# Kernel optimization log

Measured on AMD Instinct MI355X. Metric: run time of the kernel, lower is better.

## Reference

```python
import jax, jax.numpy as jnp
import numpy as np

NUM_LAYERS = 2

def setup_inputs() -> dict:
    key = jax.random.key(0)
    ks = jax.random.split(key, 10)
    N, E, V, D, G = 50000, 800000, 100000, 128, 64
    node_ids = jax.random.randint(ks[0], (N,), 0, V)
    edge_index = jax.random.randint(ks[1], (2, E), 0, N)
    batch = jnp.sort(jax.random.randint(ks[2], (N,), 0, G))
    embed = jax.random.normal(ks[3], (V, D), dtype=jnp.float32)
    conv_w = jax.random.normal(ks[4], (NUM_LAYERS, D, D), dtype=jnp.float32) * (1.0 / np.sqrt(D))
    w_ih = jax.random.normal(ks[5], (3 * D, D), dtype=jnp.float32) * (1.0 / np.sqrt(D))
    w_hh = jax.random.normal(ks[6], (3 * D, D), dtype=jnp.float32) * (1.0 / np.sqrt(D))
    b_ih = jax.random.normal(ks[7], (3 * D,), dtype=jnp.float32) * 0.01
    b_hh = jax.random.normal(ks[8], (3 * D,), dtype=jnp.float32) * 0.01
    return {"node_ids": node_ids, "edge_index": edge_index, "batch": batch,
            "num_graphs": 64, "embed": embed, "conv_w": conv_w,
            "w_ih": w_ih, "w_hh": w_hh, "b_ih": b_ih, "b_hh": b_hh}


def _gru_cell(x, h, w_ih, w_hh, b_ih, b_hh):
    # torch.nn.GRUCell math; gate order r, z, n
    gi = x @ w_ih.T + b_ih
    gh = h @ w_hh.T + b_hh
    i_r, i_z, i_n = jnp.split(gi, 3, axis=-1)
    h_r, h_z, h_n = jnp.split(gh, 3, axis=-1)
    r = jax.nn.sigmoid(i_r + h_r)
    z = jax.nn.sigmoid(i_z + h_z)
    n = jnp.tanh(i_n + r * h_n)
    return (1.0 - z) * n + z * h


def reference(node_ids, edge_index, batch, num_graphs, embed, conv_w, w_ih, w_hh, b_ih, b_hh):
    N = node_ids.shape[0]
    src, dst = edge_index[0], edge_index[1]
    h = embed[node_ids]  # [N, D]
    for i in range(NUM_LAYERS):
        m = h @ conv_w[i]                                   # [N, D]
        agg = jax.ops.segment_sum(m[src], dst, num_segments=N)  # scatter-add messages
        h = _gru_cell(agg, h, w_ih, w_hh, b_ih, b_hh)
    # global mean pool per graph
    sums = jax.ops.segment_sum(h, batch, num_segments=num_graphs)       # [G, D]
    counts = jax.ops.segment_sum(jnp.ones((N,), h.dtype), batch, num_segments=num_graphs)
    return sums / jnp.maximum(counts, 1.0)[:, None]
```

## Files before the change

### kernel.cpp

```cpp
#include <hip/hip_runtime.h>
#include <hip/hip_bf16.h>


#define DTHREADS 256

typedef __attribute__((ext_vector_type(8))) short bf16x8;
typedef __attribute__((ext_vector_type(4))) float f32x4;

__device__ __forceinline__ float sigf(float x) { return 1.0f / (1.0f + __expf(-x)); }
__device__ __forceinline__ float tanhfast(float x) { return 1.0f - 2.0f / (1.0f + __expf(2.0f * x)); }

__device__ __forceinline__ unsigned short f2bf_rne(float x) {
  unsigned int u = __float_as_uint(x);
  u += 0x7fff + ((u >> 16) & 1);
  return (unsigned short)(u >> 16);
}
__device__ __forceinline__ float bf2f(unsigned int lo16) {
  return __uint_as_float(lo16 << 16);
}

__global__ __launch_bounds__(DTHREADS) void gather_kernel(
    const float* __restrict__ embed, const int* __restrict__ node_ids,
    unsigned short* __restrict__ hb, int N) {
  int idx = blockIdx.x * DTHREADS + threadIdx.x;
  if (idx >= N * 32) return;
  int n = idx >> 5;
  int c = (idx & 31) * 4;
  int v = node_ids[n];
  float4 val = *(const float4*)&embed[(size_t)v * 128 + c];
  unsigned short b[4] = {f2bf_rne(val.x), f2bf_rne(val.y), f2bf_rne(val.z), f2bf_rne(val.w)};
  *(ushort4*)&hb[(size_t)n * 128 + c] = *(ushort4*)b;
}

#define BSHIFT 7
#define BNODES 128

__global__ __launch_bounds__(DTHREADS) void bucket_hist_kernel(
    const int* __restrict__ dst, int* __restrict__ gcnt, int E, int NB) {
  __shared__ int lc[512];
  int tid = threadIdx.x;
  for (int i = tid; i < NB; i += DTHREADS) lc[i] = 0;
  __syncthreads();
  int base = blockIdx.x * 4096;
  #pragma unroll
  for (int q = 0; q < 16; ++q) {
    int e = base + q * 256 + tid;
    if (e < E) atomicAdd(&lc[dst[e] >> BSHIFT], 1);
  }
  __syncthreads();
  for (int i = tid; i < NB; i += DTHREADS) {
    int c = lc[i];
    if (c) atomicAdd(&gcnt[i], c);
  }
}

__global__ __launch_bounds__(512) void bucket_scan_kernel(
    const int* __restrict__ gcnt, int* __restrict__ ptr, int* __restrict__ cur,
    int* __restrict__ row_ptr, int NB, int N) {
  int tid = threadIdx.x;
  int lane = tid & 63, wv = tid >> 6;
  int v = (tid < NB) ? gcnt[tid] : 0;
  int x = v;
  #pragma unroll
  for (int off = 1; off < 64; off <<= 1) {
    int y = __shfl_up(x, (unsigned)off, 64);
    if (lane >= off) x += y;
  }
  __shared__ int ws[8];
  if (lane == 63) ws[wv] = x;
  __syncthreads();
  int woff = 0;
  for (int w = 0; w < wv; ++w) woff += ws[w];
  int excl = woff + x - v;
  if (tid < NB) { ptr[tid] = excl; cur[tid] = excl; }
  if (tid == 511) { int tot = woff + x; ptr[NB] = tot; row_ptr[N] = tot; }
}

__global__ __launch_bounds__(DTHREADS) void bucket_scatter_kernel(
    const int* __restrict__ src, const int* __restrict__ dst,
    int* __restrict__ cur, unsigned int* __restrict__ ebuf, int E, int NB) {
  __shared__ int lc[512];
  __shared__ int lbs[512];
  int tid = threadIdx.x;
  for (int i = tid; i < NB; i += DTHREADS) lc[i] = 0;
  __syncthreads();
  int base = blockIdx.x * 4096;
  int rank[16];
  #pragma unroll
  for (int q = 0; q < 16; ++q) {
    int e = base + q * 256 + tid;
    if (e < E) rank[q] = atomicAdd(&lc[dst[e] >> BSHIFT], 1);
  }
  __syncthreads();
  for (int i = tid; i < NB; i += DTHREADS) {
    int c = lc[i];
    lbs[i] = c ? atomicAdd(&cur[i], c) : 0;
  }
  __syncthreads();
  #pragma unroll
  for (int q = 0; q < 16; ++q) {
    int e = base + q * 256 + tid;
    if (e < E) {
      int d = dst[e];
      unsigned int pk = (unsigned int)src[e] | ((unsigned int)(d & (BNODES - 1)) << 17);
      ebuf[lbs[d >> BSHIFT] + rank[q]] = pk;
    }
  }
}

__global__ __launch_bounds__(DTHREADS) void bucket_sort_kernel(
    const unsigned int* __restrict__ ebuf, const int* __restrict__ ptr,
    int* __restrict__ row_ptr, int* __restrict__ csr_src, int N) {
  __shared__ int cnt[BNODES];
  __shared__ int sc[BNODES];
  const int tid = threadIdx.x;
  const int b = blockIdx.x;
  const int s = ptr[b], e = ptr[b + 1];
  if (tid < BNODES) cnt[tid] = 0;
  __syncthreads();
  for (int i = s + tid; i < e; i += DTHREADS)
    atomicAdd(&cnt[ebuf[i] >> 17], 1);
  __syncthreads();
  if (tid < BNODES) sc[tid] = cnt[tid];
  __syncthreads();
  #pragma unroll
  for (int off = 1; off < BNODES; off <<= 1) {
    int t = 0;
    if (tid < BNODES && tid >= off) t = sc[tid - off];
    __syncthreads();
    if (tid < BNODES) sc[tid] += t;
    __syncthreads();
  }
  if (tid < BNODES) {
    int excl = sc[tid] - cnt[tid];
    int n = b * BNODES + tid;
    if (n < N) row_ptr[n] = s + excl;
    cnt[tid] = excl;
  }
  __syncthreads();
  for (int i = s + tid; i < e; i += DTHREADS) {
    unsigned int pk = ebuf[i];
    int slot = atomicAdd(&cnt[pk >> 17], 1);
    csr_src[s + slot] = (int)(pk & 0x1FFFFu);
  }
}

__global__ __launch_bounds__(DTHREADS) void pack_w_kernel(
    const float* __restrict__ w, unsigned short* __restrict__ wpk, int J) {
  int f = blockIdx.x * DTHREADS + threadIdx.x;
  if (f >= J * 16) return;
  int l = f & 63;
  int s = (f >> 6) & 3;
  int t = (f >> 8) & 3;
  int jb = f >> 10;
  int j = jb * 64 + t * 16 + (l & 15);
  int kb = s * 32 + (l >> 4) * 8;
  unsigned short o[8];
  #pragma unroll
  for (int i = 0; i < 8; ++i) o[i] = f2bf_rne(w[j * 128 + kb + i]);
  *(uint4*)&wpk[(size_t)f * 8] = *(uint4*)o;
}

__global__ __launch_bounds__(DTHREADS) void pack_wc_kernel(
    const float* __restrict__ conv, const float* __restrict__ w_ih,
    unsigned short* __restrict__ wpk) {
  int id = blockIdx.x * DTHREADS + threadIdx.x;
  if (id >= 384 * 128) return;
  int f = id >> 3, i = id & 7;
  int l = f & 63;
  int s = (f >> 6) & 3;
  int t = (f >> 8) & 3;
  int jb = f >> 10;
  int j = jb * 64 + t * 16 + (l & 15);
  int k = s * 32 + (l >> 4) * 8 + i;
  float acc = 0.f;
  for (int d = 0; d < 128; d += 4) {
    float4 cv = *(const float4*)&conv[k * 128 + d];
    float4 wv = *(const float4*)&w_ih[j * 128 + d];
    acc += cv.x * wv.x + cv.y * wv.y + cv.z * wv.z + cv.w * wv.w;
  }
  wpk[(size_t)f * 8 + i] = f2bf_rne(acc);
}

__global__ __launch_bounds__(DTHREADS) void aggregate_kernel(
    const unsigned short* __restrict__ hb, const int* __restrict__ row_ptr,
    const int* __restrict__ csr_src, unsigned short* __restrict__ agg, int N) {
  int w = (blockIdx.x * DTHREADS + threadIdx.x) >> 6;
  if (w >= N) return;
  int lane = threadIdx.x & 63;
  int g = lane >> 4;
  int c = lane & 15;
  int s = row_ptr[w], e = row_ptr[w + 1];
  float acc[8] = {0.f, 0.f, 0.f, 0.f, 0.f, 0.f, 0.f, 0.f};
  for (int i = s; i < e; i += 16) {
    int idx[4]; bool vl[4]; uint4 d[4];
    #pragma unroll
    for (int q = 0; q < 4; ++q) {
      int ii = i + g + q * 4;
      vl[q] = ii < e;
      idx[q] = csr_src[vl[q] ? ii : s];
    }
    #pragma unroll
    for (int q = 0; q < 4; ++q)
      d[q] = *(const uint4*)&hb[(size_t)idx[q] * 128 + c * 8];
    #pragma unroll
    for (int q = 0; q < 4; ++q) {
      if (vl[q]) {
        const unsigned int* dp = (const unsigned int*)&d[q];
        #pragma unroll
        for (int k = 0; k < 4; ++k) {
          acc[2 * k]     += bf2f(dp[k] & 0xffffu);
          acc[2 * k + 1] += bf2f(dp[k] >> 16);
        }
      }
    }
  }
  #pragma unroll
  for (int q = 0; q < 8; ++q) acc[q] += __shfl_xor(acc[q], 16, 64);
  #pragma unroll
  for (int q = 0; q < 8; ++q) acc[q] += __shfl_xor(acc[q], 32, 64);
  if (g == 0) {
    unsigned int o[4];
    #pragma unroll
    for (int q = 0; q < 4; ++q)
      o[q] = (unsigned int)f2bf_rne(acc[2 * q]) | ((unsigned int)f2bf_rne(acc[2 * q + 1]) << 16);
    *(uint4*)&agg[(size_t)w * 128 + c * 8] = *(uint4*)o;
  }
}

__global__ __launch_bounds__(512, 2) void fused_gru_kernel(
    const unsigned short* __restrict__ aggb, const unsigned short* __restrict__ wpk_wc,
    const unsigned short* __restrict__ wpk_hh, const float* __restrict__ b_ih,
    const float* __restrict__ b_hh, unsigned short* __restrict__ hb,
    int N, int nchunks) {
  __shared__ __align__(16) unsigned short Ag[32 * 128];
  __shared__ __align__(16) unsigned short Hs[32 * 128];
  const int tid = threadIdx.x;
  const int wv = tid >> 6, lane = tid & 63;
  const int lm = lane & 15, quad = lane >> 4;

  bf16x8 BI[3][4], BH[3][4];
  #pragma unroll
  for (int g = 0; g < 3; ++g) {
    int jb = g * 2 + (wv >> 2);
    int t = wv & 3;
    #pragma unroll
    for (int s = 0; s < 4; ++s) {
      size_t f = ((size_t)(jb * 4 + t) * 4 + s) * 64 + lane;
      BI[g][s] = *(const bf16x8*)&wpk_wc[f * 8];
      BH[g][s] = *(const bf16x8*)&wpk_hh[f * 8];
    }
  }

  const int jc = wv * 16 + lm;
  const float bir = b_ih[jc], biz = b_ih[128 + jc], bin_ = b_ih[256 + jc];
  const float bhr = b_hh[jc], bhz = b_hh[128 + jc], bhn = b_hh[256 + jc];
  const int c0 = jc >> 3, ej = jc & 7;

  const int srow = tid >> 4, scol = tid & 15;
  const int sdc = (scol ^ (srow & 15)) * 8;

  int ci = blockIdx.x;
  uint4 va = make_uint4(0, 0, 0, 0), vh = make_uint4(0, 0, 0, 0);
  if (ci < nchunks) {
    int n = ci * 32 + srow;
    if (n < N) {
      va = *(const uint4*)&aggb[(size_t)n * 128 + scol * 8];
      vh = *(const uint4*)&hb[(size_t)n * 128 + scol * 8];
    }
  }

  for (; ci < nchunks; ci += gridDim.x) {
    *(uint4*)&Ag[srow * 128 + sdc] = va;
    *(uint4*)&Hs[srow * 128 + sdc] = vh;
    __syncthreads();

    int cn = ci + gridDim.x;
    va = make_uint4(0, 0, 0, 0); vh = make_uint4(0, 0, 0, 0);
    if (cn < nchunks) {
      int n = cn * 32 + srow;
      if (n < N) {
        va = *(const uint4*)&aggb[(size_t)n * 128 + scol * 8];
        vh = *(const uint4*)&hb[(size_t)n * 128 + scol * 8];
      }
    }

    f32x4 accI[2][3], accH[2][3];
    #pragma unroll
    for (int mi = 0; mi < 2; ++mi)
      #pragma unroll
      for (int g = 0; g < 3; ++g) {
        accI[mi][g] = (f32x4){0.f, 0.f, 0.f, 0.f};
        accH[mi][g] = (f32x4){0.f, 0.f, 0.f, 0.f};
      }

    #pragma unroll
    for (int s = 0; s < 4; ++s) {
      bf16x8 afA[2], afH[2];
      #pragma unroll
      for (int mi = 0; mi < 2; ++mi) {
        int m = mi * 16 + lm;
        int chunk = (s * 4 + quad) ^ (m & 15);
        afA[mi] = *(const bf16x8*)&Ag[m * 128 + chunk * 8];
        afH[mi] = *(const bf16x8*)&Hs[m * 128 + chunk * 8];
      }
      #pragma unroll
      for (int g = 0; g < 3; ++g)
        #pragma unroll
        for (int mi = 0; mi < 2; ++mi) {
          accI[mi][g] = __builtin_amdgcn_mfma_f32_16x16x32_bf16(afA[mi], BI[g][s], accI[mi][g], 0, 0, 0);
          accH[mi][g] = __builtin_amdgcn_mfma_f32_16x16x32_bf16(afH[mi], BH[g][s], accH[mi][g], 0, 0, 0);
        }
    }

    const int n0 = ci * 32;
    #pragma unroll
    for (int mi = 0; mi < 2; ++mi) {
      #pragma unroll
      for (int r = 0; r < 4; ++r) {
        int row = mi * 16 + quad * 4 + r;
        int n = n0 + row;
        if (n >= N) continue;
        float ir = accI[mi][0][r] + bir;
        float iz = accI[mi][1][r] + biz;
        float in_ = accI[mi][2][r] + bin_;
        float hr = accH[mi][0][r] + bhr;
        float hz = accH[mi][1][r] + bhz;
        float hn = accH[mi][2][r] + bhn;
        float rr = sigf(ir + hr);
        float zz = sigf(iz + hz);
        float nn = tanhfast(in_ + rr * hn);
        float hold = bf2f((unsigned int)Hs[row * 128 + ((c0 ^ (row & 15)) * 8) + ej]);
        hb[(size_t)n * 128 + jc] = f2bf_rne((1.f - zz) * nn + zz * hold);
      }
    }
    __syncthreads();
  }
}

__global__ __launch_bounds__(DTHREADS) void pool1_kernel(
    const unsigned short* __restrict__ hb, const int* __restrict__ batch,
    float* __restrict__ outsum, int N) {
  int b = blockIdx.x;
  int c = threadIdx.x & 127;
  int half = threadIdx.x >> 7;
  int nbeg = b * 64;
  int nend = min(nbeg + 64, N);
  float acc = 0.f;
  int cur = -1;
  for (int n = nbeg + half; n < nend; n += 2) {
    int g = batch[n];
    if (g != cur) {
      if (cur >= 0) atomicAdd(&outsum[(size_t)cur * 128 + c], acc);
      acc = 0.f;
      cur = g;
    }
    acc += bf2f((unsigned int)hb[(size_t)n * 128 + c]);
  }
  if (cur >= 0) atomicAdd(&outsum[(size_t)cur * 128 + c], acc);
}

__device__ __forceinline__ int lbound(const int* a, int n, int key) {
  int lo = 0, hi = n;
  while (lo < hi) {
    int mid = (lo + hi) >> 1;
    if (a[mid] < key) lo = mid + 1; else hi = mid;
  }
  return lo;
}

__global__ __launch_bounds__(128) void pool2_kernel(
    const float* __restrict__ outsum, const int* __restrict__ batch,
    float* __restrict__ out, int N) {
  int g = blockIdx.x;
  int c = threadIdx.x;
  int lo = lbound(batch, N, g);
  int hi = lbound(batch, N, g + 1);
  out[(size_t)g * 128 + c] = outsum[(size_t)g * 128 + c] / (float)max(hi - lo, 1);
}

extern "C" void kernel_launch(void* const* d_in, const int* in_sizes, int n_in,
                              void* d_out, int out_size, void* d_ws, size_t ws_size,
                              hipStream_t stream) {
  const int* node_ids = (const int*)d_in[0];
  const int* edge_index = (const int*)d_in[1];
  const int* batch = (const int*)d_in[2];
  const float* embed = (const float*)d_in[4];
  const float* conv_w = (const float*)d_in[5];
  const float* w_ih = (const float*)d_in[6];
  const float* w_hh = (const float*)d_in[7];
  const float* b_ih = (const float*)d_in[8];
  const float* b_hh = (const float*)d_in[9];
  float* out = (float*)d_out;

  const int N = in_sizes[0];
  const int E = in_sizes[1] / 2;
  const int G = out_size / 128;
  const int NUM_LAYERS = in_sizes[5] / (128 * 128);
  const int NB = (N + BNODES - 1) >> BSHIFT;

  const int* e_src = edge_index;
  const int* e_dst = edge_index + E;

  char* p = (char*)d_ws;
  unsigned short* hb = (unsigned short*)p;    p += (size_t)N * 128 * 2;
  unsigned short* aggb = (unsigned short*)p;  p += (size_t)N * 128 * 2;
  float* outsum = (float*)p;                  p += (size_t)G * 128 * 4;
  unsigned short* wpk_hh = (unsigned short*)p; p += (size_t)384 * 128 * 2;
  unsigned short* wpk_wc = (unsigned short*)p; p += (size_t)NUM_LAYERS * 384 * 128 * 2;
  int* bkt_cnt = (int*)p;  p += 512 * 4;
  int* bkt_ptr = (int*)p;  p += 513 * 4;
  int* bkt_cur = (int*)p;  p += 512 * 4;
  int* row_ptr = (int*)p;  p += (size_t)(N + 1) * 4;
  unsigned int* ebuf = (unsigned int*)p;  p += (size_t)E * 4;
  int* csr_src = (int*)p;  p += (size_t)E * 4;

  const int nEB = (E + 4095) / 4096;

  hipMemsetAsync(bkt_cnt, 0, 512 * sizeof(int), stream);
  hipMemsetAsync(outsum, 0, (size_t)G * 128 * sizeof(float), stream);

  bucket_hist_kernel<<<nEB, DTHREADS, 0, stream>>>(e_dst, bkt_cnt, E, NB);
  bucket_scan_kernel<<<1, 512, 0, stream>>>(bkt_cnt, bkt_ptr, bkt_cur, row_ptr, NB, N);
  bucket_scatter_kernel<<<nEB, DTHREADS, 0, stream>>>(e_src, e_dst, bkt_cur, ebuf, E, NB);
  bucket_sort_kernel<<<NB, DTHREADS, 0, stream>>>(ebuf, bkt_ptr, row_ptr, csr_src, N);

  pack_w_kernel<<<(384 * 16 + DTHREADS - 1) / DTHREADS, DTHREADS, 0, stream>>>(w_hh, wpk_hh, 384);
  for (int L = 0; L < NUM_LAYERS; ++L)
    pack_wc_kernel<<<(384 * 128 + DTHREADS - 1) / DTHREADS, DTHREADS, 0, stream>>>(
        conv_w + (size_t)L * 128 * 128, w_ih, wpk_wc + (size_t)L * 384 * 128);

  gather_kernel<<<(N * 32 + DTHREADS - 1) / DTHREADS, DTHREADS, 0, stream>>>(embed, node_ids, hb, N);

  const int nchunks = (N + 31) / 32;
  for (int L = 0; L < NUM_LAYERS; ++L) {
    aggregate_kernel<<<((size_t)N * 64 + DTHREADS - 1) / DTHREADS, DTHREADS, 0, stream>>>(
        hb, row_ptr, csr_src, aggb, N);
    fused_gru_kernel<<<256, 512, 0, stream>>>(
        aggb, wpk_wc + (size_t)L * 384 * 128, wpk_hh, b_ih, b_hh, hb, N, nchunks);
  }

  pool1_kernel<<<(N + 63) / 64, DTHREADS, 0, stream>>>(hb, batch, outsum, N);
  pool2_kernel<<<G, 128, 0, stream>>>(outsum, batch, out, N);
}
```

Measured before the change: 296.5 us.

## Fuse neighbor aggregation into GRU layer kernel with ping-pong hidden buffers

Aggregation is moved into the GRU kernel. Each wave gathers and sums neighbor rows for 4 nodes straight into shared memory, so the bf16 agg buffer no longer makes a global round trip. Hidden state ping-pongs between two buffers, since neighbors must read the old h. The weight pack kernels are merged into one launch and the outsum memset is folded into the scan kernel. The cost is that the software prefetch of the next chunk is dropped, occupancy falls to 1 block per CU with 256 blocks, and the gather is serialized inside the GEMM loop, so latency may be exposed.

New measurement: 329.4 us. 11.1% more time.

```diff
diff --git a/kernel.cpp b/kernel.cpp
--- a/kernel.cpp
+++ b/kernel.cpp
@@ -3,6 +3,8 @@
 
 
 #define DTHREADS 256
+#define BSHIFT 7
+#define BNODES 128
 
 typedef __attribute__((ext_vector_type(8))) short bf16x8;
 typedef __attribute__((ext_vector_type(4))) float f32x4;
@@ -32,9 +34,6 @@
   *(ushort4*)&hb[(size_t)n * 128 + c] = *(ushort4*)b;
 }
 
-#define BSHIFT 7
-#define BNODES 128
-
 __global__ __launch_bounds__(DTHREADS) void bucket_hist_kernel(
     const int* __restrict__ dst, int* __restrict__ gcnt, int E, int NB) {
   __shared__ int lc[512];
@@ -56,8 +55,9 @@
 
 __global__ __launch_bounds__(512) void bucket_scan_kernel(
     const int* __restrict__ gcnt, int* __restrict__ ptr, int* __restrict__ cur,
-    int* __restrict__ row_ptr, int NB, int N) {
+    int* __restrict__ row_ptr, float* __restrict__ outsum, int osz, int NB, int N) {
   int tid = threadIdx.x;
+  for (int i = tid; i < osz; i += 512) outsum[i] = 0.f;
   int lane = tid & 63, wv = tid >> 6;
   int v = (tid < NB) ? gcnt[tid] : 0;
   int x = v;
@@ -145,93 +145,45 @@
   }
 }
 
-__global__ __launch_bounds__(DTHREADS) void pack_w_kernel(
-    const float* __restrict__ w, unsigned short* __restrict__ wpk, int J) {
-  int f = blockIdx.x * DTHREADS + threadIdx.x;
-  if (f >= J * 16) return;
-  int l = f & 63;
-  int s = (f >> 6) & 3;
-  int t = (f >> 8) & 3;
-  int jb = f >> 10;
-  int j = jb * 64 + t * 16 + (l & 15);
-  int kb = s * 32 + (l >> 4) * 8;
-  unsigned short o[8];
-  #pragma unroll
-  for (int i = 0; i < 8; ++i) o[i] = f2bf_rne(w[j * 128 + kb + i]);
-  *(uint4*)&wpk[(size_t)f * 8] = *(uint4*)o;
-}
-
-__global__ __launch_bounds__(DTHREADS) void pack_wc_kernel(
-    const float* __restrict__ conv, const float* __restrict__ w_ih,
-    unsigned short* __restrict__ wpk) {
+__global__ __launch_bounds__(DTHREADS) void pack_all_kernel(
+    const float* __restrict__ w_hh, const float* __restrict__ conv_w,
+    const float* __restrict__ w_ih, unsigned short* __restrict__ wpk_hh,
+    unsigned short* __restrict__ wpk_wc, int nl) {
   int id = blockIdx.x * DTHREADS + threadIdx.x;
-  if (id >= 384 * 128) return;
-  int f = id >> 3, i = id & 7;
+  int seg = id / (384 * 128);
+  if (seg > nl) return;
+  int r = id - seg * (384 * 128);
+  int f = r >> 3, i = r & 7;
   int l = f & 63;
   int s = (f >> 6) & 3;
   int t = (f >> 8) & 3;
   int jb = f >> 10;
   int j = jb * 64 + t * 16 + (l & 15);
   int k = s * 32 + (l >> 4) * 8 + i;
-  float acc = 0.f;
-  for (int d = 0; d < 128; d += 4) {
-    float4 cv = *(const float4*)&conv[k * 128 + d];
-    float4 wv = *(const float4*)&w_ih[j * 128 + d];
-    acc += cv.x * wv.x + cv.y * wv.y + cv.z * wv.z + cv.w * wv.w;
-  }
-  wpk[(size_t)f * 8 + i] = f2bf_rne(acc);
-}
-
-__global__ __launch_bounds__(DTHREADS) void aggregate_kernel(
-    const unsigned short* __restrict__ hb, const int* __restrict__ row_ptr,
-    const int* __restrict__ csr_src, unsigned short* __restrict__ agg, int N) {
-  int w = (blockIdx.x * DTHREADS + threadIdx.x) >> 6;
-  if (w >= N) return;
-  int lane = threadIdx.x & 63;
-  int g = lane >> 4;
-  int c = lane & 15;
-  int s = row_ptr[w], e = row_ptr[w + 1];
-  float acc[8] = {0.f, 0.f, 0.f, 0.f, 0.f, 0.f, 0.f, 0.f};
-  for (int i = s; i < e; i += 16) {
-    int idx[4]; bool vl[4]; uint4 d[4];
-    #pragma unroll
-    for (int q = 0; q < 4; ++q) {
-      int ii = i + g + q * 4;
-      vl[q] = ii < e;
-      idx[q] = csr_src[vl[q] ? ii : s];
-    }
-    #pragma unroll
-    for (int q = 0; q < 4; ++q)
-      d[q] = *(const uint4*)&hb[(size_t)idx[q] * 128 + c * 8];
-    #pragma unroll
-    for (int q = 0; q < 4; ++q) {
-      if (vl[q]) {
-        const unsigned int* dp = (const unsigned int*)&d[q];
-        #pragma unroll
-        for (int k = 0; k < 4; ++k) {
-          acc[2 * k]     += bf2f(dp[k] & 0xffffu);
-          acc[2 * k + 1] += bf2f(dp[k] >> 16);
-        }
-      }
-    }
-  }
-  #pragma unroll
-  for (int q = 0; q < 8; ++q) acc[q] += __shfl_xor(acc[q], 16, 64);
-  #pragma unroll
-  for (int q = 0; q < 8; ++q) acc[q] += __shfl_xor(acc[q], 32, 64);
-  if (g == 0) {
-    unsigned int o[4];
-    #pragma unroll
-    for (int q = 0; q < 4; ++q)
-      o[q] = (unsigned int)f2bf_rne(acc[2 * q]) | ((unsigned int)f2bf_rne(acc[2 * q + 1]) << 16);
-    *(uint4*)&agg[(size_t)w * 128 + c * 8] = *(uint4*)o;
-  }
-}
-
-__global__ __launch_bounds__(512, 2) void fused_gru_kernel(
-    const unsigned short* __restrict__ aggb, const unsigned short* __restrict__ wpk_wc,
-    const unsigned short* __restrict__ wpk_hh, const float* __restrict__ b_ih,
-    const float* __restrict__ b_hh, unsigned short* __restrict__ hb,
+  float val;
+  unsigned short* dst;
+  if (seg == 0) {
+    val = w_hh[j * 128 + k];
+    dst = wpk_hh;
+  } else {
+    const float* conv = conv_w + (size_t)(seg - 1) * 128 * 128;
+    float acc = 0.f;
+    for (int d = 0; d < 128; d += 4) {
+      float4 cv = *(const float4*)&conv[k * 128 + d];
+      float4 wv = *(const float4*)&w_ih[j * 128 + d];
+      acc += cv.x * wv.x + cv.y * wv.y + cv.z * wv.z + cv.w * wv.w;
+    }
+    val = acc;
+    dst = wpk_wc + (size_t)(seg - 1) * 384 * 128;
+  }
+  dst[(size_t)f * 8 + i] = f2bf_rne(val);
+}
+
+__global__ __launch_bounds__(512, 1) void layer_kernel(
+    const unsigned short* __restrict__ hin, unsigned short* __restrict__ hout,
+    const int* __restrict__ row_ptr, const int* __restrict__ csr_src,
+    const unsigned short* __restrict__ wpk_wc, const unsigned short* __restrict__ wpk_hh,
+    const float* __restrict__ b_ih, const float* __restrict__ b_hh,
     int N, int nchunks) {
   __shared__ __align__(16) unsigned short Ag[32 * 128];
   __shared__ __align__(16) unsigned short Hs[32 * 128];
@@ -260,30 +212,83 @@
   const int srow = tid >> 4, scol = tid & 15;
   const int sdc = (scol ^ (srow & 15)) * 8;
 
-  int ci = blockIdx.x;
-  uint4 va = make_uint4(0, 0, 0, 0), vh = make_uint4(0, 0, 0, 0);
-  if (ci < nchunks) {
-    int n = ci * 32 + srow;
-    if (n < N) {
-      va = *(const uint4*)&aggb[(size_t)n * 128 + scol * 8];
-      vh = *(const uint4*)&hb[(size_t)n * 128 + scol * 8];
-    }
-  }
-
-  for (; ci < nchunks; ci += gridDim.x) {
-    *(uint4*)&Ag[srow * 128 + sdc] = va;
-    *(uint4*)&Hs[srow * 128 + sdc] = vh;
+  for (int ci = blockIdx.x; ci < nchunks; ci += gridDim.x) {
+    const int n0 = ci * 32;
+
+    {
+      int n = n0 + srow;
+      uint4 vh = make_uint4(0, 0, 0, 0);
+      if (n < N) vh = *(const uint4*)&hin[(size_t)n * 128 + scol * 8];
+      *(uint4*)&Hs[srow * 128 + sdc] = vh;
+    }
+    {
+      const int nb = n0 + wv * 4;
+      int s0[4], e0[4];
+      #pragma unroll
+      for (int k = 0; k < 4; ++k) {
+        int n = nb + k;
+        s0[k] = (n < N) ? row_ptr[n] : 0;
+        e0[k] = (n < N) ? row_ptr[n + 1] : 0;
+      }
+      float acc[4][8];
+      #pragma unroll
+      for (int k = 0; k < 4; ++k)
+        #pragma unroll
+        for (int q = 0; q < 8; ++q) acc[k][q] = 0.f;
+      int maxd = 0;
+      #pragma unroll
+      for (int k = 0; k < 4; ++k) maxd = max(maxd, e0[k] - s0[k]);
+
+      for (int off = 0; off < maxd; off += 16) {
+        int idx[4][4];
+        #pragma unroll
+        for (int k = 0; k < 4; ++k)
+          #pragma unroll
+          for (int q = 0; q < 4; ++q) {
+            int ii = s0[k] + off + quad + q * 4;
+            idx[k][q] = (ii < e0[k]) ? csr_src[ii] : csr_src[0];
+          }
+        uint4 d[4][4];
+        #pragma unroll
+        for (int k = 0; k < 4; ++k)
+          #pragma unroll
+          for (int q = 0; q < 4; ++q)
+            d[k][q] = *(const uint4*)&hin[(size_t)idx[k][q] * 128 + lm * 8];
+        #pragma unroll
+        for (int k = 0; k < 4; ++k)
+          #pragma unroll
+          for (int q = 0; q < 4; ++q) {
+            if (s0[k] + off + quad + q * 4 < e0[k]) {
+              const unsigned int* dp = (const unsigned int*)&d[k][q];
+              #pragma unroll
+              for (int u = 0; u < 4; ++u) {
+                acc[k][2 * u]     += bf2f(dp[u] & 0xffffu);
+                acc[k][2 * u + 1] += bf2f(dp[u] >> 16);
+              }
+            }
+          }
+      }
+      #pragma unroll
+      for (int k = 0; k < 4; ++k) {
+        #pragma unroll
+        for (int q = 0; q < 8; ++q) acc[k][q] += __shfl_xor(acc[k][q], 16, 64);
+        #pragma unroll
+        for (int q = 0; q < 8; ++q) acc[k][q] += __shfl_xor(acc[k][q], 32, 64);
+      }
+      if (quad == 0) {
+        #pragma unroll
+        for (int k = 0; k < 4; ++k) {
+          int row = wv * 4 + k;
+          unsigned int o[4];
+          #pragma unroll
+          for (int q = 0; q < 4; ++q)
+            o[q] = (unsigned int)f2bf_rne(acc[k][2 * q]) |
+                   ((unsigned int)f2bf_rne(acc[k][2 * q + 1]) << 16);
+          *(uint4*)&Ag[row * 128 + ((lm ^ (row & 15)) * 8)] = *(uint4*)o;
+        }
+      }
+    }
     __syncthreads();
-
-    int cn = ci + gridDim.x;
-    va = make_uint4(0, 0, 0, 0); vh = make_uint4(0, 0, 0, 0);
-    if (cn < nchunks) {
-      int n = cn * 32 + srow;
-      if (n < N) {
-        va = *(const uint4*)&aggb[(size_t)n * 128 + scol * 8];
-        vh = *(const uint4*)&hb[(size_t)n * 128 + scol * 8];
-      }
-    }
 
     f32x4 accI[2][3], accH[2][3];
     #pragma unroll
@@ -293,7 +298,6 @@
         accI[mi][g] = (f32x4){0.f, 0.f, 0.f, 0.f};
         accH[mi][g] = (f32x4){0.f, 0.f, 0.f, 0.f};
       }
-
     #pragma unroll
     for (int s = 0; s < 4; ++s) {
       bf16x8 afA[2], afH[2];
@@ -313,13 +317,13 @@
         }
     }
 
-    const int n0 = ci * 32;
+    const int nb0 = n0;
     #pragma unroll
     for (int mi = 0; mi < 2; ++mi) {
       #pragma unroll
       for (int r = 0; r < 4; ++r) {
         int row = mi * 16 + quad * 4 + r;
-        int n = n0 + row;
+        int n = nb0 + row;
         if (n >= N) continue;
         float ir = accI[mi][0][r] + bir;
         float iz = accI[mi][1][r] + biz;
@@ -331,7 +335,7 @@
         float zz = sigf(iz + hz);
         float nn = tanhfast(in_ + rr * hn);
         float hold = bf2f((unsigned int)Hs[row * 128 + ((c0 ^ (row & 15)) * 8) + ej]);
-        hb[(size_t)n * 128 + jc] = f2bf_rne((1.f - zz) * nn + zz * hold);
+        hout[(size_t)n * 128 + jc] = f2bf_rne((1.f - zz) * nn + zz * hold);
       }
     }
     __syncthreads();
@@ -403,8 +407,8 @@
   const int* e_dst = edge_index + E;
 
   char* p = (char*)d_ws;
-  unsigned short* hb = (unsigned short*)p;    p += (size_t)N * 128 * 2;
-  unsigned short* aggb = (unsigned short*)p;  p += (size_t)N * 128 * 2;
+  unsigned short* hb0 = (unsigned short*)p;   p += (size_t)N * 128 * 2;
+  unsigned short* hb1 = (unsigned short*)p;   p += (size_t)N * 128 * 2;
   float* outsum = (float*)p;                  p += (size_t)G * 128 * 4;
   unsigned short* wpk_hh = (unsigned short*)p; p += (size_t)384 * 128 * 2;
   unsigned short* wpk_wc = (unsigned short*)p; p += (size_t)NUM_LAYERS * 384 * 128 * 2;
@@ -418,28 +422,31 @@
   const int nEB = (E + 4095) / 4096;
 
   hipMemsetAsync(bkt_cnt, 0, 512 * sizeof(int), stream);
-  hipMemsetAsync(outsum, 0, (size_t)G * 128 * sizeof(float), stream);
 
   bucket_hist_kernel<<<nEB, DTHREADS, 0, stream>>>(e_dst, bkt_cnt, E, NB);
-  bucket_scan_kernel<<<1, 512, 0, stream>>>(bkt_cnt, bkt_ptr, bkt_cur, row_ptr, NB, N);
+  bucket_scan_kernel<<<1, 512, 0, stream>>>(bkt_cnt, bkt_ptr, bkt_cur, row_ptr,
+                                            outsum, G * 128, NB, N);
   bucket_scatter_kernel<<<nEB, DTHREADS, 0, stream>>>(e_src, e_dst, bkt_cur, ebuf, E, NB);
   bucket_sort_kernel<<<NB, DTHREADS, 0, stream>>>(ebuf, bkt_ptr, row_ptr, csr_src, N);
 
-  pack_w_kernel<<<(384 * 16 + DTHREADS - 1) / DTHREADS, DTHREADS, 0, stream>>>(w_hh, wpk_hh, 384);
-  for (int L = 0; L < NUM_LAYERS; ++L)
-    pack_wc_kernel<<<(384 * 128 + DTHREADS - 1) / DTHREADS, DTHREADS, 0, stream>>>(
-        conv_w + (size_t)L * 128 * 128, w_ih, wpk_wc + (size_t)L * 384 * 128);
-
-  gather_kernel<<<(N * 32 + DTHREADS - 1) / DTHREADS, DTHREADS, 0, stream>>>(embed, node_ids, hb, N);
+  {
+    int total = (NUM_LAYERS + 1) * 384 * 128;
+    pack_all_kernel<<<(total + DTHREADS - 1) / DTHREADS, DTHREADS, 0, stream>>>(
+        w_hh, conv_w, w_ih, wpk_hh, wpk_wc, NUM_LAYERS);
+  }
+
+  gather_kernel<<<(N * 32 + DTHREADS - 1) / DTHREADS, DTHREADS, 0, stream>>>(embed, node_ids, hb0, N);
 
   const int nchunks = (N + 31) / 32;
   for (int L = 0; L < NUM_LAYERS; ++L) {
-    aggregate_kernel<<<((size_t)N * 64 + DTHREADS - 1) / DTHREADS, DTHREADS, 0, stream>>>(
-        hb, row_ptr, csr_src, aggb, N);
-    fused_gru_kernel<<<256, 512, 0, stream>>>(
-        aggb, wpk_wc + (size_t)L * 384 * 128, wpk_hh, b_ih, b_hh, hb, N, nchunks);
-  }
-
-  pool1_kernel<<<(N + 63) / 64, DTHREADS, 0, stream>>>(hb, batch, outsum, N);
+    const unsigned short* hin = (L % 2 == 0) ? hb0 : hb1;
+    unsigned short* hout = (L % 2 == 0) ? hb1 : hb0;
+    layer_kernel<<<256, 512, 0, stream>>>(
+        hin, hout, row_ptr, csr_src, wpk_wc + (size_t)L * 384 * 128, wpk_hh,
+        b_ih, b_hh, N, nchunks);
+  }
+
+  const unsigned short* hfin = (NUM_LAYERS % 2 == 0) ? hb0 : hb1;
+  pool1_kernel<<<(N + 63) / 64, DTHREADS, 0, stream>>>(hfin, batch, outsum, N);
   pool2_kernel<<<G, 128, 0, stream>>>(outsum, batch, out, N);
 }
```
